# Kernel optimization log

Measured on AMD Instinct MI355X. Metric: run time of the kernel, lower is better.

## Reference

```python
import math
import jax, jax.numpy as jnp
import numpy as np

B, T, C, H = 2, 2048, 768, 12
D = C // H
EPS = 1e-5


def setup_inputs() -> dict:
    key = jax.random.key(0)
    ks = jax.random.split(key, 12)
    s = 0.02
    return {
        "x": jax.random.normal(ks[0], (B, T, C), jnp.float32),
        "Wqkv": jax.random.normal(ks[1], (C, 3 * C), jnp.float32) * s,
        "bqkv": jnp.zeros((3 * C,), jnp.float32),
        "Wo": jax.random.normal(ks[2], (C, C), jnp.float32) * s,
        "bo": jnp.zeros((C,), jnp.float32),
        "ln1_g": jnp.ones((C,), jnp.float32),
        "ln1_b": jnp.zeros((C,), jnp.float32),
        "Wf": jax.random.normal(ks[3], (C, 4 * C), jnp.float32) * s,
        "bf": jnp.zeros((4 * C,), jnp.float32),
        "Wp": jax.random.normal(ks[4], (4 * C, C), jnp.float32) * s,
        "bp": jnp.zeros((C,), jnp.float32),
        "ln2_g": jnp.ones((C,), jnp.float32),
        "ln2_b": jnp.zeros((C,), jnp.float32),
    }


def _layernorm(x, g, b):
    mu = jnp.mean(x, axis=-1, keepdims=True)
    var = jnp.mean(jnp.square(x - mu), axis=-1, keepdims=True)
    return (x - mu) * jax.lax.rsqrt(var + EPS) * g + b


def _attention(x, Wqkv, bqkv):
    qkv = x @ Wqkv + bqkv                      # [B,T,3C]
    q, k, v = jnp.split(qkv, 3, axis=-1)
    q = q.reshape(B, T, H, D)
    k = k.reshape(B, T, H, D)
    v = v.reshape(B, T, H, D)
    # scores: [B,H,T,T] -- deliberately materialized as in the source module
    scores = jnp.einsum('bqhd,bkhd->bhqk', q, k) / math.sqrt(D)
    causal = jnp.tril(jnp.ones((T, T), bool))
    scores = jnp.where(causal, scores, -jnp.inf)
    w = jax.nn.softmax(scores, axis=-1)
    out = jnp.einsum('bhqk,bkhd->bqhd', w, v)
    return out.reshape(B, T, C)


def reference(x, Wqkv, bqkv, Wo, bo, ln1_g, ln1_b, Wf, bf, Wp, bp, ln2_g, ln2_b):
    # attention skip + post-LN
    h = x + _attention(x, Wqkv, bqkv) @ Wo + bo
    h = _layernorm(h, ln1_g, ln1_b)
    # GELU (exact, erf-based, matching nn.GELU default) FFN skip + post-LN
    h = h + jax.nn.gelu(h @ Wf + bf, approximate=False) @ Wp + bp
    h = _layernorm(h, ln2_g, ln2_b)
    return h
```

## Files before the change

### kernel.cpp

```cpp
#include <hip/hip_runtime.h>

#define BB 2
#define TT 2048
#define CC 768
#define HH 12
#define DD 64
#define TBT (BB * TT)

typedef __bf16 bfx8 __attribute__((ext_vector_type(8)));
typedef float f32x4 __attribute__((ext_vector_type(4)));
typedef float f32x16 __attribute__((ext_vector_type(16)));

__device__ __forceinline__ unsigned short f2b(float f) {
  unsigned u = __float_as_uint(f);
  return (unsigned short)((u + 0x7FFFu + ((u >> 16) & 1u)) >> 16);
}
__device__ __forceinline__ float b2f(unsigned short u) {
  return __uint_as_float(((unsigned)u) << 16);
}

__device__ __forceinline__ unsigned pack2bf(float lo, float hi) {
  union { __bf16 h[2]; unsigned u; } x;
  x.h[0] = (__bf16)lo; x.h[1] = (__bf16)hi;
  return x.u;
}

__device__ __forceinline__ void gload_lds16(const void* g, void* l) {
  __builtin_amdgcn_global_load_lds((const __attribute__((address_space(1))) void*)g,
                                   (__attribute__((address_space(3))) void*)l, 16, 0, 0);
}

__device__ __forceinline__ float gelu_fast(float v) {
  float t = v * v;
  float s = fmaf(0.10294663f, t, 2.3021582f);
  float e = __builtin_amdgcn_exp2f(-v * s);
  return v * __builtin_amdgcn_rcpf(1.0f + e);
}

__global__ __launch_bounds__(256) void k_prep(const float* __restrict__ x,
                                              unsigned short* __restrict__ xb,
                                              const float* __restrict__ Wqkv,
                                              unsigned short* __restrict__ WqkvT,
                                              const float* __restrict__ Wo,
                                              unsigned short* __restrict__ WoT,
                                              const float* __restrict__ Wf,
                                              unsigned short* __restrict__ WfT,
                                              const float* __restrict__ Wp,
                                              unsigned short* __restrict__ WpT) {
  __shared__ float tile[32][33];
  int bid = blockIdx.x;
  const int tid = threadIdx.x;
  if (bid < 3072) {
    int i = bid * 1024 + tid * 4;
    float4 v = *(const float4*)(x + i);
    ushort4 o;
    o.x = f2b(v.x); o.y = f2b(v.y); o.z = f2b(v.z); o.w = f2b(v.w);
    *(ushort4*)(xb + i) = o;
    return;
  }
  bid -= 3072;
  const float* W; unsigned short* WT; int K, N, bx, by;
  if (bid < 1728)              { W = Wqkv; WT = WqkvT; K = 768;  N = 2304; bx = bid % 72; by = bid / 72; }
  else if (bid < 1728 + 576)   { bid -= 1728; W = Wo; WT = WoT; K = 768;  N = 768;  bx = bid % 24; by = bid / 24; }
  else if (bid < 1728 + 576 + 2304) { bid -= 1728 + 576; W = Wf; WT = WfT; K = 768; N = 3072; bx = bid % 96; by = bid / 96; }
  else                         { bid -= 1728 + 576 + 2304; W = Wp; WT = WpT; K = 3072; N = 768; bx = bid % 24; by = bid / 24; }
  int n0 = bx * 32, k0 = by * 32;
  int j = tid & 31, i0 = tid >> 5;
  for (int i = i0; i < 32; i += 8) tile[i][j] = W[(size_t)(k0 + i) * N + n0 + j];
  __syncthreads();
  for (int i = i0; i < 32; i += 8) WT[(size_t)(n0 + i) * K + k0 + j] = f2b(tile[j][i]);
}

template<int MODE>
__global__ __launch_bounds__(256) void k_gemm_bt(const unsigned short* __restrict__ A,
                                                 const unsigned short* __restrict__ Bt,
                                                 const float* __restrict__ bias,
                                                 unsigned short* __restrict__ outb,
                                                 unsigned short* __restrict__ vt,
                                                 float* __restrict__ outf0,
                                                 float* __restrict__ outf1,
                                                 int M, int N, int K) {
  __shared__ __align__(16) unsigned short SMEM[4][128 * 64];
  const int tid = threadIdx.x;
  const int l = tid & 63, w = tid >> 6;
  const int wr = w >> 1, wc = w & 1;
  const int lr = l & 15, g = l >> 4;

  const int gx = gridDim.x, nwg = gx * gridDim.y;
  const int orig = blockIdx.x + gx * blockIdx.y;
  const int q8 = nwg >> 3;
  const int swz = (orig & 7) * q8 + (orig >> 3);
  const int m0 = (swz / gx) * 128, n0 = (swz % gx) * 128;

  int kbeg = 0, kend = K;
  if (MODE == 3) { int K2 = K >> 1; kbeg = blockIdx.z * K2; kend = kbeg + K2; }

  f32x4 acc[4][4] = {};

  auto stage = [&](int kt, int buf) {
#pragma unroll
    for (int i = 0; i < 4; ++i) {
      int s = tid + i * 256;
      int row = s >> 3;
      int q = (s & 7) ^ (row & 7);
      gload_lds16(A + (size_t)(m0 + row) * K + kt + q * 8, &SMEM[buf][s * 8]);
      gload_lds16(Bt + (size_t)(n0 + row) * K + kt + q * 8, &SMEM[2 + buf][s * 8]);
    }
  };

  stage(kbeg, 0);
  __syncthreads();

  int cur = 0;
  for (int kt = kbeg; kt < kend; kt += 64) {
    if (kt + 64 < kend) stage(kt + 64, cur ^ 1);
    const unsigned short* As = &SMEM[cur][0];
    const unsigned short* Bs = &SMEM[2 + cur][0];
#pragma unroll
    for (int kk = 0; kk < 2; ++kk) {
      bfx8 af[4], bfr[4];
#pragma unroll
      for (int m = 0; m < 4; ++m) {
        int row = wr * 64 + m * 16 + lr;
        int quad = (kk * 4 + g) ^ (row & 7);
        af[m] = *(const bfx8*)(&As[row * 64 + quad * 8]);
      }
#pragma unroll
      for (int n = 0; n < 4; ++n) {
        int row = wc * 64 + n * 16 + lr;
        int quad = (kk * 4 + g) ^ (row & 7);
        bfr[n] = *(const bfx8*)(&Bs[row * 64 + quad * 8]);
      }
#pragma unroll
      for (int m = 0; m < 4; ++m)
#pragma unroll
        for (int n = 0; n < 4; ++n)
          acc[m][n] = __builtin_amdgcn_mfma_f32_16x16x32_bf16(af[m], bfr[n], acc[m][n], 0, 0, 0);
    }
    __syncthreads();
    cur ^= 1;
  }

  if (MODE == 0 && n0 >= 2 * CC) {
    unsigned short* T = &SMEM[0][0];
#pragma unroll
    for (int m = 0; m < 4; ++m)
#pragma unroll
      for (int n = 0; n < 4; ++n) {
        int tcol = wc * 64 + n * 16 + lr;
        float bv = bias[n0 + tcol];
#pragma unroll
        for (int r = 0; r < 4; ++r) {
          int trow = wr * 64 + m * 16 + g * 4 + r;
          T[tcol * 128 + (trow ^ ((tcol & 15) << 3))] = f2b(acc[m][n][r] + bv);
        }
      }
    __syncthreads();
    int tcol = tid >> 1, half = tid & 1;
    int gcol = n0 - 2 * CC + tcol;
    int hh = gcol >> 6, dd = gcol & 63;
    int bloc = m0 >> 11;
    int tb = m0 & 2047;
    unsigned short* dstrow = vt + ((size_t)(bloc * HH + hh) * DD + dd) * TT + tb;
#pragma unroll
    for (int c = 0; c < 8; ++c) {
      int tbase = half * 64 + c * 8;
      bfx8 val = *(const bfx8*)(&T[tcol * 128 + (tbase ^ ((tcol & 15) << 3))]);
      *(bfx8*)(dstrow + tbase) = val;
    }
    return;
  }

  float* dst = (MODE == 3) ? (blockIdx.z ? outf1 : outf0) : nullptr;
#pragma unroll
  for (int m = 0; m < 4; ++m) {
#pragma unroll
    for (int n = 0; n < 4; ++n) {
      int col = n0 + wc * 64 + n * 16 + lr;
      float bv = (MODE == 3) ? 0.f : bias[col];
#pragma unroll
      for (int r = 0; r < 4; ++r) {
        int row = m0 + wr * 64 + m * 16 + g * 4 + r;
        float v = acc[m][n][r] + bv;
        if (MODE == 1) v = gelu_fast(v);
        if (MODE == 3) {
          dst[(size_t)row * N + col] = v;
        } else {
          outb[(size_t)row * N + col] = f2b(v);
        }
      }
    }
  }
}

#define MFIX 8.0f
__global__ __launch_bounds__(256) void k_attn(const unsigned short* __restrict__ qkv,
                                              const unsigned short* __restrict__ VT,
                                              unsigned short* __restrict__ aout,
                                              unsigned short* __restrict__ opart,
                                              float* __restrict__ lbuf) {
  __shared__ __align__(16) unsigned short Ks[3][64 * 64];
  __shared__ __align__(16) unsigned short Vs[3][64 * 64];
  const int tid = threadIdx.x;
  const int l = tid & 63, w = tid >> 6;
  const int ql = l & 31, hi = l >> 5;
  const int bh = blockIdx.y;
  const int b = bh / HH, h = bh % HH;

  const int cid = blockIdx.x;
  int bx, sub;
  if (cid < 4)       { bx = cid;                  sub = 0; }
  else if (cid < 12) { bx = 4 + ((cid - 4) >> 1); sub = (cid - 4) & 1; }
  else if (cid < 24) { bx = 8 + (cid - 12) / 3;   sub = (cid - 12) % 3; }
  else               { bx = 12 + ((cid - 24) >> 2); sub = (cid - 24) & 3; }
  const int nt = 2 * bx + 2;
  const int nchunks = (nt + 7) >> 3;
  const int t0i = sub * 8;
  const int tcount = min(8, nt - t0i);

  const int qw = bx * 128 + w * 32;
  const int qrow = qw + ql;

  const unsigned short* Kbase = qkv + (size_t)(b * TT) * (3 * CC) + CC + h * DD;
  const unsigned short* Vbase = VT + (size_t)bh * DD * TT;

  bfx8 qf[4];
  {
    const unsigned short* qp = qkv + (size_t)(b * TT + qrow) * (3 * CC) + h * DD;
    const float SC = 0.125f * 1.44269504088896340736f;
#pragma unroll
    for (int c = 0; c < 4; ++c) {
      bfx8 rw = *(const bfx8*)(qp + c * 16 + hi * 8);
#pragma unroll
      for (int j = 0; j < 8; ++j) qf[c][j] = (__bf16)((float)rw[j] * SC);
    }
  }

  f32x16 o0 = {}, o1 = {};
  float l_run = 0.f;

  auto stage = [&](int t, int bufi) {
    const int k0 = t * 64;
#pragma unroll
    for (int i = 0; i < 2; ++i) {
      int sl = tid + i * 256;
      int row = sl >> 3;
      int q = (sl & 7) ^ (row & 7);
      gload_lds16(Kbase + (size_t)(k0 + row) * (3 * CC) + q * 8, &Ks[bufi][sl * 8]);
      gload_lds16(Vbase + (size_t)row * TT + k0 + q * 8, &Vs[bufi][sl * 8]);
    }
  };

  stage(t0i, 0);
  stage(t0i + 1, 1);
  asm volatile("s_waitcnt vmcnt(4)" ::: "memory");
  __builtin_amdgcn_sched_barrier(0);
  __builtin_amdgcn_s_barrier();

  int cb = 0;
  int sb = 2;
  for (int ti = 0; ti < tcount; ++ti) {
    if (ti + 2 < tcount) stage(t0i + ti + 2, sb);

    const int t = t0i + ti;
    const int k0 = t * 64;
    if (k0 <= qw + 31) {
      f32x16 sa[2];
      __builtin_amdgcn_s_setprio(1);
#pragma unroll
      for (int kh = 0; kh < 2; ++kh) {
        f32x16 acc = {};
        int row = kh * 32 + ql;
        int rx = row & 7;
#pragma unroll
        for (int c = 0; c < 4; ++c) {
          int quad = (c * 2 + hi) ^ rx;
          bfx8 kf = *(const bfx8*)(&Ks[cb][row * 64 + quad * 8]);
          acc = __builtin_amdgcn_mfma_f32_32x32x16_bf16(kf, qf[c], acc, 0, 0, 0);
        }
        sa[kh] = acc;
      }
      __builtin_amdgcn_s_setprio(0);

      if (k0 + 63 > qw) {
#pragma unroll
        for (int kh = 0; kh < 2; ++kh)
#pragma unroll
          for (int r = 0; r < 16; ++r) {
            int kk = k0 + kh * 32 + (r & 3) + 8 * (r >> 2) + 4 * hi;
            if (kk > qrow) sa[kh][r] = -1e30f;
          }
      }

      float rs0 = 0.f, rs1 = 0.f, rs2 = 0.f, rs3 = 0.f;
      unsigned pk[2][8];
#pragma unroll
      for (int kh = 0; kh < 2; ++kh)
#pragma unroll
        for (int i = 0; i < 8; ++i) {
          float p0 = __builtin_amdgcn_exp2f(sa[kh][2 * i] - MFIX);
          float p1 = __builtin_amdgcn_exp2f(sa[kh][2 * i + 1] - MFIX);
          float ps = p0 + p1;
          if ((i & 3) == 0) rs0 += ps;
          else if ((i & 3) == 1) rs1 += ps;
          else if ((i & 3) == 2) rs2 += ps;
          else rs3 += ps;
          pk[kh][i] = pack2bf(p0, p1);
        }
      float rs = (rs0 + rs1) + (rs2 + rs3);
      rs += __shfl_xor(rs, 32);
      l_run += rs;

      bfx8 pf[4];
#pragma unroll
      for (int kh = 0; kh < 2; ++kh)
#pragma unroll
        for (int c = 0; c < 2; ++c) {
          unsigned a0 = pk[kh][c * 4 + 0], a1 = pk[kh][c * 4 + 1];
          unsigned b0 = pk[kh][c * 4 + 2], b1 = pk[kh][c * 4 + 3];
          asm volatile("v_permlane32_swap_b32 %0, %1" : "+v"(a0), "+v"(b0));
          asm volatile("v_permlane32_swap_b32 %0, %1" : "+v"(a1), "+v"(b1));
          union { unsigned u[4]; bfx8 v; } cvt;
          cvt.u[0] = a0; cvt.u[1] = a1; cvt.u[2] = b0; cvt.u[3] = b1;
          pf[kh * 2 + c] = cvt.v;
        }

      __builtin_amdgcn_s_setprio(1);
#pragma unroll
      for (int kc = 0; kc < 4; ++kc) {
        {
          int row = ql;
          bfx8 vf = *(const bfx8*)(&Vs[cb][row * 64 + (((kc * 2 + hi) ^ (row & 7)) * 8)]);
          o0 = __builtin_amdgcn_mfma_f32_32x32x16_bf16(vf, pf[kc], o0, 0, 0, 0);
        }
        {
          int row = 32 + ql;
          bfx8 vf = *(const bfx8*)(&Vs[cb][row * 64 + (((kc * 2 + hi) ^ (row & 7)) * 8)]);
          o1 = __builtin_amdgcn_mfma_f32_32x32x16_bf16(vf, pf[kc], o1, 0, 0, 0);
        }
      }
      __builtin_amdgcn_s_setprio(0);
    }

    if (ti + 2 < tcount) {
      asm volatile("s_waitcnt vmcnt(4)" ::: "memory");
    } else {
      asm volatile("s_waitcnt vmcnt(0)" ::: "memory");
    }
    __builtin_amdgcn_sched_barrier(0);
    __builtin_amdgcn_s_barrier();

    cb = (cb == 2) ? 0 : cb + 1;
    sb = (sb == 2) ? 0 : sb + 1;
  }

  if (nchunks == 1) {
    float inv = 1.0f / l_run;
    unsigned short* orow = aout + (size_t)(b * TT + qrow) * CC + h * DD;
#pragma unroll
    for (int dh = 0; dh < 2; ++dh) {
      const f32x16& oo = dh ? o1 : o0;
#pragma unroll
      for (int qd = 0; qd < 4; ++qd) {
        ushort4 v;
        v.x = f2b(oo[qd * 4 + 0] * inv);
        v.y = f2b(oo[qd * 4 + 1] * inv);
        v.z = f2b(oo[qd * 4 + 2] * inv);
        v.w = f2b(oo[qd * 4 + 3] * inv);
        *(ushort4*)(orow + dh * 32 + 8 * qd + 4 * hi) = v;
      }
    }
  } else {
    unsigned short* orow = opart + (size_t)sub * TBT * CC + (size_t)(b * TT + qrow) * CC + h * DD;
#pragma unroll
    for (int dh = 0; dh < 2; ++dh) {
      const f32x16& oo = dh ? o1 : o0;
#pragma unroll
      for (int qd = 0; qd < 4; ++qd) {
        ushort4 v;
        v.x = f2b(oo[qd * 4 + 0]);
        v.y = f2b(oo[qd * 4 + 1]);
        v.z = f2b(oo[qd * 4 + 2]);
        v.w = f2b(oo[qd * 4 + 3]);
        *(ushort4*)(orow + dh * 32 + 8 * qd + 4 * hi) = v;
      }
    }
    if (hi == 0) lbuf[((size_t)sub * (BB * HH) + bh) * TT + qrow] = l_run;
  }
}

__global__ __launch_bounds__(256) void k_attn_combine(const unsigned short* __restrict__ opart,
                                                      const float* __restrict__ lbuf,
                                                      unsigned short* __restrict__ aout) {
  int idx = (blockIdx.x * 256 + threadIdx.x) * 4;
  int bt = idx / CC, c = idx % CC;
  int b = bt >> 11, t = bt & (TT - 1);
  int bx = t >> 7;
  int cnt = (2 * bx + 9) >> 3;
  if (cnt < 2) return;
  int h = c >> 6;
  int bh = b * HH + h;

  float lsum = 0.f;
#pragma unroll
  for (int s = 0; s < 4; ++s)
    if (s < cnt) lsum += lbuf[((size_t)s * (BB * HH) + bh) * TT + t];
  float linv = 1.0f / lsum;

  float a0 = 0.f, a1 = 0.f, a2 = 0.f, a3 = 0.f;
#pragma unroll
  for (int s = 0; s < 4; ++s)
    if (s < cnt) {
      ushort4 v = *(const ushort4*)(opart + (size_t)s * TBT * CC + idx);
      a0 += b2f(v.x);
      a1 += b2f(v.y);
      a2 += b2f(v.z);
      a3 += b2f(v.w);
    }
  ushort4 o;
  o.x = f2b(a0 * linv);
  o.y = f2b(a1 * linv);
  o.z = f2b(a2 * linv);
  o.w = f2b(a3 * linv);
  *(ushort4*)(aout + idx) = o;
}

template<int WF32, int WB16>
__global__ __launch_bounds__(256) void k_layernorm_c(const float* __restrict__ in0,
                                                     const float* __restrict__ in1,
                                                     const float* __restrict__ resid,
                                                     const float* __restrict__ biasv,
                                                     const float* __restrict__ gw,
                                                     const float* __restrict__ bw,
                                                     float* __restrict__ outf,
                                                     unsigned short* __restrict__ outb) {
  __shared__ float red[8];
  const int row = blockIdx.x;
  const int tid = threadIdx.x;
  float v[3];
  float s = 0.f;
#pragma unroll
  for (int j = 0; j < 3; ++j) {
    int c = tid + j * 256;
    size_t idx = (size_t)row * CC + c;
    v[j] = in0[idx] + in1[idx] + resid[idx] + biasv[c];
    s += v[j];
  }
#pragma unroll
  for (int off = 32; off; off >>= 1) s += __shfl_xor(s, off);
  if ((tid & 63) == 0) red[tid >> 6] = s;
  __syncthreads();
  s = red[0] + red[1] + red[2] + red[3];
  float mu = s * (1.0f / CC);
  float qs = 0.f;
#pragma unroll
  for (int j = 0; j < 3; ++j) { float d = v[j] - mu; qs += d * d; }
#pragma unroll
  for (int off = 32; off; off >>= 1) qs += __shfl_xor(qs, off);
  if ((tid & 63) == 0) red[4 + (tid >> 6)] = qs;
  __syncthreads();
  qs = red[4] + red[5] + red[6] + red[7];
  float rstd = rsqrtf(qs * (1.0f / CC) + 1e-5f);
#pragma unroll
  for (int j = 0; j < 3; ++j) {
    int c = tid + j * 256;
    float y = (v[j] - mu) * rstd * gw[c] + bw[c];
    if (WF32) outf[(size_t)row * CC + c] = y;
    if (WB16) outb[(size_t)row * CC + c] = f2b(y);
  }
}

extern "C" void kernel_launch(void* const* d_in, const int* in_sizes, int n_in,
                              void* d_out, int out_size, void* d_ws, size_t ws_size,
                              hipStream_t stream) {
  (void)in_sizes; (void)n_in; (void)out_size; (void)ws_size;
  const float* x    = (const float*)d_in[0];
  const float* Wqkv = (const float*)d_in[1];
  const float* bqkv = (const float*)d_in[2];
  const float* Wo   = (const float*)d_in[3];
  const float* bo   = (const float*)d_in[4];
  const float* ln1g = (const float*)d_in[5];
  const float* ln1b = (const float*)d_in[6];
  const float* Wf   = (const float*)d_in[7];
  const float* bf_  = (const float*)d_in[8];
  const float* Wp   = (const float*)d_in[9];
  const float* bp   = (const float*)d_in[10];
  const float* ln2g = (const float*)d_in[11];
  const float* ln2b = (const float*)d_in[12];

  char* ws = (char*)d_ws;
  size_t off = 0;
  auto alloc = [&](size_t bytes) {
    void* p = ws + off;
    off += (bytes + 255) & ~(size_t)255;
    return p;
  };
  unsigned short* xb    = (unsigned short*)alloc((size_t)TBT * CC * 2);
  unsigned short* WqkvT = (unsigned short*)alloc((size_t)3 * CC * CC * 2);
  unsigned short* WoT   = (unsigned short*)alloc((size_t)CC * CC * 2);
  unsigned short* WfT   = (unsigned short*)alloc((size_t)4 * CC * CC * 2);
  unsigned short* WpT   = (unsigned short*)alloc((size_t)4 * CC * CC * 2);
  unsigned short* qkvb  = (unsigned short*)alloc((size_t)TBT * 3 * CC * 2);
  unsigned short* VTb   = (unsigned short*)alloc((size_t)TBT * CC * 2);
  float*          hbuf  = (float*)alloc((size_t)TBT * CC * 4);
  float*          hln   = (float*)alloc((size_t)TBT * CC * 4);
  unsigned short* hlnb  = (unsigned short*)alloc((size_t)TBT * CC * 2);
  unsigned short* gbuf  = (unsigned short*)alloc((size_t)TBT * 4 * CC * 2);

  unsigned short* aout  = xb;
  unsigned short* opart = gbuf;
  float*          lvals = (float*)hbuf;
  float*          woP0  = (float*)gbuf;
  float*          woP1  = (float*)((char*)gbuf + (size_t)TBT * CC * 4);
  float*          fpP0  = hbuf;
  float*          fpP1  = (float*)qkvb;

  k_prep<<<9984, 256, 0, stream>>>(x, xb, Wqkv, WqkvT, Wo, WoT, Wf, WfT, Wp, WpT);

  k_gemm_bt<0><<<dim3(3 * CC / 128, TBT / 128), 256, 0, stream>>>(
      xb, WqkvT, bqkv, qkvb, VTb, nullptr, nullptr, TBT, 3 * CC, CC);
  k_attn<<<dim3(40, BB * HH), 256, 0, stream>>>(qkvb, VTb, aout, opart, lvals);
  k_attn_combine<<<(TBT * CC) / 1024, 256, 0, stream>>>(opart, lvals, aout);
  k_gemm_bt<3><<<dim3(CC / 128, TBT / 128, 2), 256, 0, stream>>>(
      aout, WoT, nullptr, nullptr, nullptr, woP0, woP1, TBT, CC, CC);
  k_layernorm_c<1, 1><<<TBT, 256, 0, stream>>>(woP0, woP1, x, bo, ln1g, ln1b, hln, hlnb);
  k_gemm_bt<1><<<dim3(4 * CC / 128, TBT / 128), 256, 0, stream>>>(
      hlnb, WfT, bf_, gbuf, nullptr, nullptr, nullptr, TBT, 4 * CC, CC);
  k_gemm_bt<3><<<dim3(CC / 128, TBT / 128, 2), 256, 0, stream>>>(
      gbuf, WpT, nullptr, nullptr, nullptr, fpP0, fpP1, TBT, CC, 4 * CC);
  k_layernorm_c<1, 0><<<TBT, 256, 0, stream>>>(fpP0, fpP1, hln, bp, ln2g, ln2b,
                                               (float*)d_out, nullptr);
}
```

Before: 178.7 us.

## Stage GEMM epilogue through swizzled LDS for vector stores; reorder attention blocks

The GEMM epilogue now writes accumulators into XOR-swizzled shared memory and then emits row-contiguous 16-byte vector stores to global memory, replacing scattered scalar stores. Both the fp32 split-K output and the bf16 output paths use this. The attention kernel replaces its arithmetic block-to-work mapping with lookup tables that put heavy blocks first, improving load balance. The cost is an extra LDS round trip and a barrier per tile.

Result: slower. 201.5 us (+12.8%).

```diff
diff --git a/kernel.cpp b/kernel.cpp
--- a/kernel.cpp
+++ b/kernel.cpp
@@ -171,29 +171,65 @@
     return;
   }
 
-  float* dst = (MODE == 3) ? (blockIdx.z ? outf1 : outf0) : nullptr;
-#pragma unroll
-  for (int m = 0; m < 4; ++m) {
-#pragma unroll
-    for (int n = 0; n < 4; ++n) {
-      int col = n0 + wc * 64 + n * 16 + lr;
-      float bv = (MODE == 3) ? 0.f : bias[col];
-#pragma unroll
-      for (int r = 0; r < 4; ++r) {
-        int row = m0 + wr * 64 + m * 16 + g * 4 + r;
-        float v = acc[m][n][r] + bv;
-        if (MODE == 1) v = gelu_fast(v);
-        if (MODE == 3) {
-          dst[(size_t)row * N + col] = v;
-        } else {
-          outb[(size_t)row * N + col] = f2b(v);
-        }
-      }
+  if (MODE == 3) {
+    float* T = (float*)&SMEM[0][0];
+#pragma unroll
+    for (int m = 0; m < 4; ++m)
+#pragma unroll
+      for (int n = 0; n < 4; ++n) {
+        int col = wc * 64 + n * 16 + lr;
+#pragma unroll
+        for (int r = 0; r < 4; ++r) {
+          int row = wr * 64 + m * 16 + g * 4 + r;
+          T[row * 128 + (col ^ ((row & 7) << 2))] = acc[m][n][r];
+        }
+      }
+    __syncthreads();
+    float* dst = blockIdx.z ? outf1 : outf0;
+    int row = tid >> 1, half = tid & 1;
+    float* gptr = dst + (size_t)(m0 + row) * N + n0 + half * 64;
+    const int s = (row & 7) << 2;
+#pragma unroll
+    for (int j = 0; j < 16; ++j) {
+      f32x4 v = *(const f32x4*)&T[row * 128 + ((half * 64 + j * 4) ^ s)];
+      *(f32x4*)(gptr + j * 4) = v;
+    }
+    return;
+  }
+
+  {
+    unsigned short* T = &SMEM[0][0];
+#pragma unroll
+    for (int m = 0; m < 4; ++m)
+#pragma unroll
+      for (int n = 0; n < 4; ++n) {
+        int col = wc * 64 + n * 16 + lr;
+        float bv = bias[n0 + col];
+#pragma unroll
+        for (int r = 0; r < 4; ++r) {
+          int row = wr * 64 + m * 16 + g * 4 + r;
+          float v = acc[m][n][r] + bv;
+          if (MODE == 1) v = gelu_fast(v);
+          T[row * 128 + (col ^ ((row & 7) << 3))] = f2b(v);
+        }
+      }
+    __syncthreads();
+    int row = tid >> 1, half = tid & 1;
+    unsigned short* gptr = outb + (size_t)(m0 + row) * N + n0 + half * 64;
+    const int s = (row & 7) << 3;
+#pragma unroll
+    for (int j = 0; j < 8; ++j) {
+      bfx8 v = *(const bfx8*)&T[row * 128 + ((half * 64 + j * 8) ^ s)];
+      *(bfx8*)(gptr + j * 8) = v;
     }
   }
 }
 
 #define MFIX 8.0f
+__device__ const unsigned char CBX[40]  = {3,4,5,6,7,7,8,8,9,9,10,10,11,11,11,12,12,12,13,13,13,14,14,14,15,15,15,15,
+                                           2,6,10,14, 1,5,9,13, 0,4,8,12};
+__device__ const unsigned char CSUB[40] = {0,0,0,0,0,1,0,1,0,1,0,1,0,1,2,0,1,2,0,1,2,0,1,2,0,1,2,3,
+                                           0,1,2,3, 0,1,2,3, 0,1,2,3};
 __global__ __launch_bounds__(256) void k_attn(const unsigned short* __restrict__ qkv,
                                               const unsigned short* __restrict__ VT,
                                               unsigned short* __restrict__ aout,
@@ -207,12 +243,8 @@
   const int bh = blockIdx.y;
   const int b = bh / HH, h = bh % HH;
 
-  const int cid = blockIdx.x;
-  int bx, sub;
-  if (cid < 4)       { bx = cid;                  sub = 0; }
-  else if (cid < 12) { bx = 4 + ((cid - 4) >> 1); sub = (cid - 4) & 1; }
-  else if (cid < 24) { bx = 8 + (cid - 12) / 3;   sub = (cid - 12) % 3; }
-  else               { bx = 12 + ((cid - 24) >> 2); sub = (cid - 24) & 3; }
+  const int bx = CBX[blockIdx.x];
+  const int sub = CSUB[blockIdx.x];
   const int nt = 2 * bx + 2;
   const int nchunks = (nt + 7) >> 3;
   const int t0i = sub * 8;
```
